# Kernel optimization log

Hardware: AMD Instinct MI355X
Metric: run time of the kernel (lower is better)

The kernel has to match this reference:

```python
import jax, jax.numpy as jnp
import numpy as np

N = 16384   # nodes
K = 10      # knn_graph(k=11) minus self-loop -> 10 neighbors per node
H = 128     # hidden_nf
L = 7       # n_layers
IN = 8      # in_node_nf
OUT = 4     # out_node_nf


def setup_inputs() -> dict:
    key = jax.random.key(0)
    ks = jax.random.split(key, 20)
    s = 0.05
    rn = lambda k, shp, sc=s: (jax.random.normal(k, shp, dtype=jnp.float32) * sc)
    return {
        "h": jax.random.normal(ks[0], (N, 3 + IN), dtype=jnp.float32) * 100.0,  # cols 0:3 coords (divided by 3330 inside), 3: features
        "idx": jax.random.randint(ks[1], (N, K), 0, N),  # neighbor (src) indices per dst node
        "emb_in_w": rn(ks[2], (IN, H)), "emb_in_b": rn(ks[3], (H,)),
        "edge_w1": rn(ks[4], (L, 2 * H + 1, H)), "edge_b1": rn(ks[5], (L, H)),
        "edge_w2": rn(ks[6], (L, H, H)), "edge_b2": rn(ks[7], (L, H)),
        "coord_w1": rn(ks[8], (L, H, H)), "coord_b1": rn(ks[9], (L, H)),
        "coord_w2": rn(ks[10], (L, H, 1), 0.001),  # xavier gain=0.001, no bias
        "node_w1": rn(ks[11], (L, 2 * H, H)), "node_b1": rn(ks[12], (L, H)),
        "node_w2": rn(ks[13], (L, H, H)), "node_b2": rn(ks[14], (L, H)),
        "emb_out_w": rn(ks[15], (H + 3, OUT)), "emb_out_b": rn(ks[16], (OUT,)),
        "step_count": 0,
    }


def reference(h, idx, emb_in_w, emb_in_b, edge_w1, edge_b1, edge_w2, edge_b2,
              coord_w1, coord_b1, coord_w2, node_w1, node_b1, node_w2, node_b2,
              emb_out_w, emb_out_b, step_count):
    silu = jax.nn.silu
    x = h[:, :3] / 3330.0                       # [N,3] coordinates
    hh = h[:, 3:] @ emb_in_w + emb_in_b         # [N,H] embedding_in (plain Linear)
    for l in range(edge_w1.shape[0]):           # 7 E_GCL layers (structurally distinct params)
        # --- RelativePositionCordMessage (per-edge, edges = (idx[i,k] -> i)) ---
        x_s = x[idx]                            # [N,K,3] src coords (gather)
        hh_s = hh[idx]                          # [N,K,H] src features (gather)
        diff = x_s - x[:, None, :]              # src - dst
        radial = jnp.sum(diff * diff, axis=-1, keepdims=True)   # [N,K,1]
        hh_d = jnp.broadcast_to(hh[:, None, :], hh_s.shape)
        ef = jnp.concatenate([radial, hh_s, hh_d], axis=-1)     # [N,K,2H+1]
        ef = silu(ef @ edge_w1[l] + edge_b1[l])
        ef = silu(ef @ edge_w2[l] + edge_b2[l])                 # edge_feature [N,K,H]
        cm = silu(ef @ coord_w1[l] + coord_b1[l]) @ coord_w2[l] # [N,K,1] (no bias, no tanh)
        trans = diff * cm                                        # [N,K,3]
        # --- Aggregationlayer (mailbox mean/sum reduce + node MLP) ---
        trans = jnp.clip(trans, -1000.0, 1000.0)
        x = jnp.clip(x, -1000.0, 1000.0) + jnp.mean(trans, axis=1)
        agg = jnp.concatenate([hh, jnp.sum(ef, axis=1)], axis=-1)  # [N,2H]
        dh = silu(agg @ node_w1[l] + node_b1[l]) @ node_w2[l] + node_b2[l]
        hh = hh + dh                                              # residual=True
    out = jnp.concatenate([hh, x], axis=-1) @ emb_out_w + emb_out_b  # embedding_out [N,4]
    return out
```

## Files before the change

### kernel.cpp

```cpp
#include <hip/hip_runtime.h>
#include <hip/hip_bf16.h>

#define NN 16384
#define KNN 10
#define HD 128
#define NL 7
#define TM 8
#define EDG 80

#define W1E_OFF 0
#define W1D_OFF 16384
#define W2_OFF  32768
#define C1_OFF  49152
#define N1_OFF  65536
#define N2_OFF  98304
#define WL_STRIDE 114688

typedef float fv4 __attribute__((ext_vector_type(4)));
typedef short bv8 __attribute__((ext_vector_type(8)));

static __device__ __forceinline__ unsigned short f2b(float f) {
  __hip_bfloat16 h = __float2bfloat16(f);
  return __builtin_bit_cast(unsigned short, h);
}
static __device__ __forceinline__ float b2f(unsigned short u) {
  unsigned int x = ((unsigned int)u) << 16;
  return __builtin_bit_cast(float, x);
}
static __device__ __forceinline__ unsigned int pk2(float lo, float hi) {
  unsigned int r;
  asm("v_cvt_pk_bf16_f32 %0, %1, %2" : "=v"(r) : "v"(lo), "v"(hi));
  return r;
}
static __device__ __forceinline__ float silu_f(float x) {
  return x * __builtin_amdgcn_rcpf(1.0f + __expf(-x));
}
#define MFMA(a,b,c) __builtin_amdgcn_mfma_f32_16x16x32_bf16((a),(b),(c),0,0,0)

static __device__ __forceinline__ int swz8(int row, int col) {
  return row * 128 + (col ^ ((row & 7) << 3));
}

__global__ void prep_kernel(const float* __restrict__ ew1, const float* __restrict__ ew2,
                            const float* __restrict__ cw1, const float* __restrict__ nw1,
                            const float* __restrict__ nw2, unsigned short* __restrict__ wt)
{
  int g = blockIdx.x * 256 + threadIdx.x;
  if (g >= NL * WL_STRIDE) return;
  int l = g / WL_STRIDE;
  int r = g % WL_STRIDE;
  float v;
  if (r < 16384) {
    int c = r >> 7, k = r & 127;
    v = ew1[(l*257 + 1 + k)*128 + c];
  } else if (r < 32768) {
    int q = r - 16384; int c = q >> 7, k = q & 127;
    v = ew1[(l*257 + 129 + k)*128 + c];
  } else if (r < 49152) {
    int q = r - 32768; int c = q >> 7, k = q & 127;
    v = ew2[(l*128 + k)*128 + c];
  } else if (r < 65536) {
    int q = r - 49152; int c = q >> 7, k = q & 127;
    v = cw1[(l*128 + k)*128 + c];
  } else if (r < 98304) {
    int q = r - 65536; int c = q >> 8, k = q & 255;
    v = nw1[(l*256 + k)*128 + c];
  } else {
    int q = r - 98304; int c = q >> 7, k = q & 127;
    v = nw2[(l*128 + k)*128 + c];
  }
  wt[g] = f2b(v);
}

__global__ void init_kernel(const float* __restrict__ h, const float* __restrict__ eiw,
                            const float* __restrict__ eib, float* __restrict__ hh,
                            unsigned short* __restrict__ hhb, float* __restrict__ x)
{
  int g = blockIdx.x * 256 + threadIdx.x;
  int n = g >> 7, c = g & 127;
  float acc = eib[c];
  #pragma unroll
  for (int j = 0; j < 8; ++j) acc += h[n*11 + 3 + j] * eiw[j*128 + c];
  hh[g] = acc;
  hhb[g] = f2b(acc);
  if (c < 3) x[n*4 + c] = h[n*11 + c] * (1.0f/3330.0f);
  if (c == 3) x[n*4 + 3] = 0.f;
}

__global__ void out_kernel(const float* __restrict__ hh, const float* __restrict__ x,
                           const float* __restrict__ ow, const float* __restrict__ ob,
                           float* __restrict__ out)
{
  int g = blockIdx.x * 256 + threadIdx.x;
  int n = g >> 2, o = g & 3;
  float acc = ob[o];
  #pragma unroll 8
  for (int k = 0; k < 128; ++k) acc += hh[n*128 + k] * ow[k*4 + o];
  #pragma unroll
  for (int d = 0; d < 3; ++d) acc += x[n*4 + d] * ow[(128 + d)*4 + o];
  out[g] = acc;
}

static __device__ __forceinline__ void load_w8(bv8* w, const unsigned short* __restrict__ W,
                                               int cwb, int lr, int lh) {
  #pragma unroll
  for (int ks = 0; ks < 4; ++ks) {
    w[ks]     = *(const bv8*)(W + (cwb      + lr)*128 + ks*32 + lh*8);
    w[4 + ks] = *(const bv8*)(W + (cwb + 16 + lr)*128 + ks*32 + lh*8);
  }
}

__global__ __launch_bounds__(256, 3) void layer_kernel(
    const int* __restrict__ idxp,
    const unsigned short* __restrict__ wt,
    const float* __restrict__ eb1, const float* __restrict__ eb2,
    const float* __restrict__ cb1, const float* __restrict__ cw2,
    const float* __restrict__ nb1, const float* __restrict__ nb2,
    const float* __restrict__ w1r0p,
    float* __restrict__ hh,
    const unsigned short* __restrict__ hhbin,
    unsigned short* __restrict__ hhbout,
    const float* __restrict__ xin, float* __restrict__ xout)
{
  __shared__ __align__(16) unsigned char smem[49792];
  unsigned short* sA   = (unsigned short*)(smem);
  unsigned short* sB   = (unsigned short*)(smem + 20480);
  float*          sHC  = (float*)(smem + 40960);
  unsigned short* sAg  = (unsigned short*)(smem + 45184);
  float*          sCmP = (float*)(smem + 47232);
  float* sRad = (float*)(smem + 48512);
  float* sDx  = (float*)(smem + 48832);
  float* sDy  = (float*)(smem + 49152);
  float* sDz  = (float*)(smem + 49472);
  unsigned short* sEf = sA;
  unsigned short* sN1 = sB;

  const int tid  = threadIdx.x;
  const int wave = tid >> 6;
  const int lane = tid & 63;
  const int lr   = lane & 15;
  const int lh   = lane >> 4;
  const int cwb  = wave * 32;
  const int cb0  = cwb + lh*4;
  const int node0 = blockIdx.x * TM;

  bv8 hb[4];
  #pragma unroll
  for (int ks = 0; ks < 4; ++ks)
    hb[ks] = *(const bv8*)(hhbin + (node0 + (lr & 7))*HD + ks*32 + lh*8);
  bv8 wd[8]; load_w8(wd, wt + W1D_OFF, cwb, lr, lh);
  fv4 cw2v0 = *(const fv4*)(cw2 + cb0);
  fv4 cw2v1 = *(const fv4*)(cw2 + cb0 + 16);
  fv4 w1r0v0 = *(const fv4*)(w1r0p + cb0);
  fv4 w1r0v1 = *(const fv4*)(w1r0p + cb0 + 16);

  if (tid < EDG) {
    int e = tid, n = e / KNN;
    int s = idxp[node0*KNN + e];
    fv4 xs4 = *(const fv4*)(xin + s*4);
    fv4 xd4 = *(const fv4*)(xin + (node0+n)*4);
    float d0 = xs4[0]-xd4[0], d1 = xs4[1]-xd4[1], d2 = xs4[2]-xd4[2];
    sDx[e] = d0; sDy[e] = d1; sDz[e] = d2;
    sRad[e] = d0*d0 + d1*d1 + d2*d2;
  }
  #pragma unroll
  for (int it = 0; it < 5; ++it) {
    int q = tid + it*256;
    int e = q >> 4, c = (q & 15) << 3;
    int s = idxp[node0*KNN + e];
    bv8 v = *(const bv8*)(hhbin + s*HD + c);
    *(bv8*)(sA + swz8(e, c)) = v;
  }
  {
    fv4 hac[2];
    hac[0] = *(const fv4*)(eb1 + cb0);
    hac[1] = *(const fv4*)(eb1 + cb0 + 16);
    #pragma unroll
    for (int ks = 0; ks < 4; ++ks) {
      hac[0] = MFMA(wd[ks],   hb[ks], hac[0]);
      hac[1] = MFMA(wd[4+ks], hb[ks], hac[1]);
    }
    if (lr < TM) {
      *(fv4*)(sHC + lr*132 + cb0)      = hac[0];
      *(fv4*)(sHC + lr*132 + cb0 + 16) = hac[1];
    }
  }
  bv8 we[8]; load_w8(we, wt + W1E_OFF, cwb, lr, lh);
  __syncthreads();

  bv8 w2r[8]; load_w8(w2r, wt + W2_OFF, cwb, lr, lh);
  {
    fv4 acc[5][2];
    #pragma unroll
    for (int n = 0; n < 5; ++n) {
      int e = n*16 + lr;
      int nd = e / KNN;
      float rad = sRad[e];
      fv4 h0 = *(const fv4*)(sHC + nd*132 + cb0);
      fv4 h1 = *(const fv4*)(sHC + nd*132 + cb0 + 16);
      acc[n][0] = h0 + w1r0v0*rad;
      acc[n][1] = h1 + w1r0v1*rad;
    }
    #pragma unroll
    for (int ks = 0; ks < 4; ++ks) {
      #pragma unroll
      for (int n = 0; n < 5; ++n) {
        bv8 b = *(const bv8*)(sA + swz8(n*16 + lr, ks*32 + lh*8));
        acc[n][0] = MFMA(we[ks],   b, acc[n][0]);
        acc[n][1] = MFMA(we[4+ks], b, acc[n][1]);
      }
    }
    #pragma unroll
    for (int n = 0; n < 5; ++n) {
      int e = n*16 + lr;
      #pragma unroll
      for (int mt = 0; mt < 2; ++mt) {
        uint2 p;
        p.x = pk2(silu_f(acc[n][mt][0]), silu_f(acc[n][mt][1]));
        p.y = pk2(silu_f(acc[n][mt][2]), silu_f(acc[n][mt][3]));
        *(uint2*)(sB + swz8(e, cb0 + mt*16)) = p;
      }
    }
  }
  __syncthreads();

  bv8 c1r[8]; load_w8(c1r, wt + C1_OFF, cwb, lr, lh);
  {
    fv4 bb0 = *(const fv4*)(eb2 + cb0);
    fv4 bb1 = *(const fv4*)(eb2 + cb0 + 16);
    fv4 acc[5][2];
    #pragma unroll
    for (int n = 0; n < 5; ++n) { acc[n][0] = bb0; acc[n][1] = bb1; }
    #pragma unroll
    for (int ks = 0; ks < 4; ++ks) {
      #pragma unroll
      for (int n = 0; n < 5; ++n) {
        bv8 b = *(const bv8*)(sB + swz8(n*16 + lr, ks*32 + lh*8));
        acc[n][0] = MFMA(w2r[ks],   b, acc[n][0]);
        acc[n][1] = MFMA(w2r[4+ks], b, acc[n][1]);
      }
    }
    #pragma unroll
    for (int n = 0; n < 5; ++n) {
      int e = n*16 + lr;
      #pragma unroll
      for (int mt = 0; mt < 2; ++mt) {
        uint2 p;
        p.x = pk2(silu_f(acc[n][mt][0]), silu_f(acc[n][mt][1]));
        p.y = pk2(silu_f(acc[n][mt][2]), silu_f(acc[n][mt][3]));
        *(uint2*)(sA + swz8(e, cb0 + mt*16)) = p;
      }
    }
  }
  __syncthreads();

  bv8 n1r[16];
  #pragma unroll
  for (int ks = 0; ks < 8; ++ks)
    n1r[ks] = *(const bv8*)(wt + N1_OFF + (cwb + lr)*256 + ks*32 + lh*8);
  {
    fv4 bb0 = *(const fv4*)(cb1 + cb0);
    fv4 bb1 = *(const fv4*)(cb1 + cb0 + 16);
    fv4 acc[5][2];
    #pragma unroll
    for (int n = 0; n < 5; ++n) { acc[n][0] = bb0; acc[n][1] = bb1; }
    #pragma unroll
    for (int ks = 0; ks < 4; ++ks) {
      #pragma unroll
      for (int n = 0; n < 5; ++n) {
        bv8 b = *(const bv8*)(sEf + swz8(n*16 + lr, ks*32 + lh*8));
        acc[n][0] = MFMA(c1r[ks],   b, acc[n][0]);
        acc[n][1] = MFMA(c1r[4+ks], b, acc[n][1]);
      }
    }
    if (tid >= 128) {
      int q = tid - 128;
      int n = q >> 4, c = (q & 15) << 3;
      float s[8] = {0,0,0,0,0,0,0,0};
      #pragma unroll
      for (int k = 0; k < KNN; ++k) {
        bv8 v = *(const bv8*)(sEf + swz8(n*KNN + k, c));
        #pragma unroll
        for (int e8 = 0; e8 < 8; ++e8) s[e8] += b2f((unsigned short)v[e8]);
      }
      uint4 pv = make_uint4(pk2(s[0], s[1]), pk2(s[2], s[3]),
                            pk2(s[4], s[5]), pk2(s[6], s[7]));
      *(uint4*)(sAg + swz8(n, c)) = pv;
    }
    #pragma unroll
    for (int ks = 0; ks < 8; ++ks)
      n1r[8 + ks] = *(const bv8*)(wt + N1_OFF + (cwb + 16 + lr)*256 + ks*32 + lh*8);
    #pragma unroll
    for (int n = 0; n < 5; ++n) {
      float pm = 0.f;
      #pragma unroll
      for (int j = 0; j < 4; ++j) {
        pm += silu_f(acc[n][0][j]) * cw2v0[j];
        pm += silu_f(acc[n][1][j]) * cw2v1[j];
      }
      pm += __shfl_xor(pm, 16);
      pm += __shfl_xor(pm, 32);
      if (lane < 16) sCmP[wave*80 + n*16 + lr] = pm;
    }
  }
  __syncthreads();

  bv8 n2r[8]; load_w8(n2r, wt + N2_OFF, cwb, lr, lh);
  {
    fv4 acc[2];
    acc[0] = *(const fv4*)(nb1 + cb0);
    acc[1] = *(const fv4*)(nb1 + cb0 + 16);
    #pragma unroll
    for (int ks = 0; ks < 8; ++ks) {
      bv8 b = (ks < 4) ? hb[ks]
                       : *(const bv8*)(sAg + swz8(lr & 7, (ks-4)*32 + lh*8));
      acc[0] = MFMA(n1r[ks],   b, acc[0]);
      acc[1] = MFMA(n1r[8+ks], b, acc[1]);
    }
    if (wave == 0) {
      if (lane < 3*TM) {
        int n = lane / 3, d = lane % 3;
        const float* sD = (d == 0) ? sDx : (d == 1) ? sDy : sDz;
        float xo = xin[(node0+n)*4 + d];
        xo = fminf(fmaxf(xo, -1000.f), 1000.f);
        float s = 0.f;
        #pragma unroll
        for (int k = 0; k < KNN; ++k) {
          int e = n*KNN + k;
          float cm = sCmP[e] + sCmP[80 + e] + sCmP[160 + e] + sCmP[240 + e];
          float tr = sD[e] * cm;
          tr = fminf(fmaxf(tr, -1000.f), 1000.f);
          s += tr;
        }
        xout[(node0+n)*4 + d] = xo + s * (1.0f/KNN);
      } else if (lane < 4*TM) {
        xout[(node0 + lane - 3*TM)*4 + 3] = 0.f;
      }
    }
    #pragma unroll
    for (int mt = 0; mt < 2; ++mt) {
      uint2 p;
      p.x = pk2(silu_f(acc[mt][0]), silu_f(acc[mt][1]));
      p.y = pk2(silu_f(acc[mt][2]), silu_f(acc[mt][3]));
      *(uint2*)(sN1 + swz8(lr, cb0 + mt*16)) = p;
    }
  }
  __syncthreads();

  {
    fv4 acc[2];
    acc[0] = *(const fv4*)(nb2 + cb0);
    acc[1] = *(const fv4*)(nb2 + cb0 + 16);
    #pragma unroll
    for (int ks = 0; ks < 4; ++ks) {
      bv8 b = *(const bv8*)(sN1 + swz8(lr, ks*32 + lh*8));
      acc[0] = MFMA(n2r[ks],   b, acc[0]);
      acc[1] = MFMA(n2r[4+ks], b, acc[1]);
    }
    if (lr < TM) {
      #pragma unroll
      for (int mt = 0; mt < 2; ++mt) {
        int g = (node0 + lr)*HD + cb0 + mt*16;
        fv4 v = *(const fv4*)(hh + g) + acc[mt];
        *(fv4*)(hh + g) = v;
        uint2 p;
        p.x = pk2(v[0], v[1]);
        p.y = pk2(v[2], v[3]);
        *(uint2*)(hhbout + g) = p;
      }
    }
  }
}

extern "C" void kernel_launch(void* const* d_in, const int* in_sizes, int n_in,
                              void* d_out, int out_size, void* d_ws, size_t ws_size,
                              hipStream_t stream)
{
  (void)in_sizes; (void)n_in; (void)out_size; (void)ws_size;
  const float* h   = (const float*)d_in[0];
  const int*   idx = (const int*)d_in[1];
  const float* eiw = (const float*)d_in[2];
  const float* eib = (const float*)d_in[3];
  const float* ew1 = (const float*)d_in[4];
  const float* eb1 = (const float*)d_in[5];
  const float* ew2 = (const float*)d_in[6];
  const float* eb2 = (const float*)d_in[7];
  const float* cw1 = (const float*)d_in[8];
  const float* cb1 = (const float*)d_in[9];
  const float* cw2 = (const float*)d_in[10];
  const float* nw1 = (const float*)d_in[11];
  const float* nb1 = (const float*)d_in[12];
  const float* nw2 = (const float*)d_in[13];
  const float* nb2 = (const float*)d_in[14];
  const float* eow = (const float*)d_in[15];
  const float* eob = (const float*)d_in[16];

  unsigned char* ws = (unsigned char*)d_ws;
  unsigned short* wt   = (unsigned short*)ws;
  float*          hh   = (float*)(ws + 1605632);
  unsigned short* hhbA = (unsigned short*)(ws + 9994240);
  unsigned short* hhbB = (unsigned short*)(ws + 14188544);
  float*          xA   = (float*)(ws + 18382848);
  float*          xB   = (float*)(ws + 18644992);

  prep_kernel<<<(NL*WL_STRIDE + 255)/256, 256, 0, stream>>>(ew1, ew2, cw1, nw1, nw2, wt);
  init_kernel<<<NN*HD/256, 256, 0, stream>>>(h, eiw, eib, hh, hhbA, xA);

  unsigned short* hbs = hhbA; unsigned short* hbd = hhbB;
  float* xs = xA; float* xd = xB;
  for (int l = 0; l < NL; ++l) {
    layer_kernel<<<NN/TM, 256, 0, stream>>>(idx, wt + (size_t)l*WL_STRIDE,
        eb1 + l*128, eb2 + l*128, cb1 + l*128, cw2 + l*128,
        nb1 + l*128, nb2 + l*128,
        ew1 + (size_t)l*257*128,
        hh, hbs, hbd, xs, xd);
    unsigned short* ht = hbs; hbs = hbd; hbd = ht;
    float* t = xs; xs = xd; xd = t;
  }
  out_kernel<<<NN*4/256, 256, 0, stream>>>(hh, xs, eow, eob, (float*)d_out);
}
```

Baseline: 476.8 us.

## Drop fp32 hidden-state buffer, keep bf16 only, and gather neighbors via direct-to-LDS loads

Removes the fp32 copy of the hidden state. The residual add now reads the bf16 hidden vector and writes only bf16, and the output kernel reads bf16 features with weights staged in shared memory. Neighbor feature gathers now use global_load_lds, which writes straight into the swizzled shared tile without passing through registers, and they are issued at kernel start to overlap with the other setup loads. This cuts per-layer global traffic and register pressure, but the residual stream now accumulates in bf16, so rounding error grows across the 7 layers.

```diff
diff --git a/kernel.cpp b/kernel.cpp
--- a/kernel.cpp
+++ b/kernel.cpp
@@ -36,6 +36,10 @@
   return x * __builtin_amdgcn_rcpf(1.0f + __expf(-x));
 }
 #define MFMA(a,b,c) __builtin_amdgcn_mfma_f32_16x16x32_bf16((a),(b),(c),0,0,0)
+
+#define GLOAD_LDS(gp, lp) \
+  __builtin_amdgcn_global_load_lds((const __attribute__((address_space(1))) void*)(gp), \
+                                   (__attribute__((address_space(3))) void*)(lp), 16, 0, 0)
 
 static __device__ __forceinline__ int swz8(int row, int col) {
   return row * 128 + (col ^ ((row & 7) << 3));
@@ -73,7 +77,7 @@
 }
 
 __global__ void init_kernel(const float* __restrict__ h, const float* __restrict__ eiw,
-                            const float* __restrict__ eib, float* __restrict__ hh,
+                            const float* __restrict__ eib,
                             unsigned short* __restrict__ hhb, float* __restrict__ x)
 {
   int g = blockIdx.x * 256 + threadIdx.x;
@@ -81,23 +85,31 @@
   float acc = eib[c];
   #pragma unroll
   for (int j = 0; j < 8; ++j) acc += h[n*11 + 3 + j] * eiw[j*128 + c];
-  hh[g] = acc;
   hhb[g] = f2b(acc);
   if (c < 3) x[n*4 + c] = h[n*11 + c] * (1.0f/3330.0f);
   if (c == 3) x[n*4 + 3] = 0.f;
 }
 
-__global__ void out_kernel(const float* __restrict__ hh, const float* __restrict__ x,
+__global__ void out_kernel(const unsigned short* __restrict__ hhb, const float* __restrict__ x,
                            const float* __restrict__ ow, const float* __restrict__ ob,
                            float* __restrict__ out)
 {
-  int g = blockIdx.x * 256 + threadIdx.x;
+  __shared__ float sOW[131*4];
+  int tid = threadIdx.x;
+  for (int i = tid; i < 131*4; i += 256) sOW[i] = ow[i];
+  __syncthreads();
+  int g = blockIdx.x * 256 + tid;
   int n = g >> 2, o = g & 3;
   float acc = ob[o];
-  #pragma unroll 8
-  for (int k = 0; k < 128; ++k) acc += hh[n*128 + k] * ow[k*4 + o];
-  #pragma unroll
-  for (int d = 0; d < 3; ++d) acc += x[n*4 + d] * ow[(128 + d)*4 + o];
+  #pragma unroll
+  for (int kk = 0; kk < 16; ++kk) {
+    bv8 v = *(const bv8*)(hhb + n*128 + kk*8);
+    #pragma unroll
+    for (int j = 0; j < 8; ++j)
+      acc += b2f((unsigned short)v[j]) * sOW[(kk*8 + j)*4 + o];
+  }
+  #pragma unroll
+  for (int d = 0; d < 3; ++d) acc += x[n*4 + d] * sOW[(128 + d)*4 + o];
   out[g] = acc;
 }
 
@@ -117,7 +129,6 @@
     const float* __restrict__ cb1, const float* __restrict__ cw2,
     const float* __restrict__ nb1, const float* __restrict__ nb2,
     const float* __restrict__ w1r0p,
-    float* __restrict__ hh,
     const unsigned short* __restrict__ hhbin,
     unsigned short* __restrict__ hhbout,
     const float* __restrict__ xin, float* __restrict__ xout)
@@ -144,6 +155,15 @@
   const int cb0  = cwb + lh*4;
   const int node0 = blockIdx.x * TM;
 
+  #pragma unroll
+  for (int it = 0; it < 5; ++it) {
+    int q = tid + it*256;
+    int e = q >> 4, cq = q & 15;
+    int s = idxp[node0*KNN + e];
+    int csw = (cq ^ (e & 7)) << 3;
+    GLOAD_LDS(hhbin + s*HD + csw, sA + ((q & ~63) << 3));
+  }
+
   bv8 hb[4];
   #pragma unroll
   for (int ks = 0; ks < 4; ++ks)
@@ -163,14 +183,6 @@
     sDx[e] = d0; sDy[e] = d1; sDz[e] = d2;
     sRad[e] = d0*d0 + d1*d1 + d2*d2;
   }
-  #pragma unroll
-  for (int it = 0; it < 5; ++it) {
-    int q = tid + it*256;
-    int e = q >> 4, c = (q & 15) << 3;
-    int s = idxp[node0*KNN + e];
-    bv8 v = *(const bv8*)(hhbin + s*HD + c);
-    *(bv8*)(sA + swz8(e, c)) = v;
-  }
   {
     fv4 hac[2];
     hac[0] = *(const fv4*)(eb1 + cb0);
@@ -306,6 +318,11 @@
   __syncthreads();
 
   bv8 n2r[8]; load_w8(n2r, wt + N2_OFF, cwb, lr, lh);
+  uint2 hres[2];
+  if (lr < TM) {
+    hres[0] = *(const uint2*)(hhbin + (node0 + lr)*HD + cb0);
+    hres[1] = *(const uint2*)(hhbin + (node0 + lr)*HD + cb0 + 16);
+  }
   {
     fv4 acc[2];
     acc[0] = *(const fv4*)(nb1 + cb0);
@@ -361,11 +378,13 @@
       #pragma unroll
       for (int mt = 0; mt < 2; ++mt) {
         int g = (node0 + lr)*HD + cb0 + mt*16;
-        fv4 v = *(const fv4*)(hh + g) + acc[mt];
-        *(fv4*)(hh + g) = v;
+        float v0 = b2f((unsigned short)(hres[mt].x))       + acc[mt][0];
+        float v1 = b2f((unsigned short)(hres[mt].x >> 16)) + acc[mt][1];
+        float v2 = b2f((unsigned short)(hres[mt].y))       + acc[mt][2];
+        float v3 = b2f((unsigned short)(hres[mt].y >> 16)) + acc[mt][3];
         uint2 p;
-        p.x = pk2(v[0], v[1]);
-        p.y = pk2(v[2], v[3]);
+        p.x = pk2(v0, v1);
+        p.y = pk2(v2, v3);
         *(uint2*)(hhbout + g) = p;
       }
     }
@@ -397,14 +416,13 @@
 
   unsigned char* ws = (unsigned char*)d_ws;
   unsigned short* wt   = (unsigned short*)ws;
-  float*          hh   = (float*)(ws + 1605632);
-  unsigned short* hhbA = (unsigned short*)(ws + 9994240);
-  unsigned short* hhbB = (unsigned short*)(ws + 14188544);
-  float*          xA   = (float*)(ws + 18382848);
-  float*          xB   = (float*)(ws + 18644992);
+  unsigned short* hhbA = (unsigned short*)(ws + 1605632);
+  unsigned short* hhbB = (unsigned short*)(ws + 5799936);
+  float*          xA   = (float*)(ws + 9994240);
+  float*          xB   = (float*)(ws + 10256384);
 
   prep_kernel<<<(NL*WL_STRIDE + 255)/256, 256, 0, stream>>>(ew1, ew2, cw1, nw1, nw2, wt);
-  init_kernel<<<NN*HD/256, 256, 0, stream>>>(h, eiw, eib, hh, hhbA, xA);
+  init_kernel<<<NN*HD/256, 256, 0, stream>>>(h, eiw, eib, hhbA, xA);
 
   unsigned short* hbs = hhbA; unsigned short* hbd = hhbB;
   float* xs = xA; float* xd = xB;
@@ -413,9 +431,9 @@
         eb1 + l*128, eb2 + l*128, cb1 + l*128, cw2 + l*128,
         nb1 + l*128, nb2 + l*128,
         ew1 + (size_t)l*257*128,
-        hh, hbs, hbd, xs, xd);
+        hbs, hbd, xs, xd);
     unsigned short* ht = hbs; hbs = hbd; hbd = ht;
     float* t = xs; xs = xd; xd = t;
   }
-  out_kernel<<<NN*4/256, 256, 0, stream>>>(hh, xs, eow, eob, (float*)d_out);
-}
+  out_kernel<<<NN*4/256, 256, 0, stream>>>(hbs, xs, eow, eob, (float*)d_out);
+}
```

Measured after the change: 474.4 us. Within noise of the previous version (-0.5%).
